# Kernel optimization log

Measured on AMD Instinct MI355X. Metric: run time of the kernel, lower is better.

## Reference

```python
import jax, jax.numpy as jnp
import numpy as np

B, S, D = 512, 81, 1024
NH, DH = 16, 64
C, H1, G, FF = 32, 256, 256, 4096


def _ln(x, g, b, eps=1e-5):
    m = x.mean(-1, keepdims=True)
    v = ((x - m) ** 2).mean(-1, keepdims=True)
    return (x - m) * jax.lax.rsqrt(v + eps) * g + b


def _mish(x):
    return x * jnp.tanh(jax.nn.softplus(x))


def setup_inputs() -> dict:
    key = jax.random.key(0)
    ks = iter(jax.random.split(key, 32))
    n = lambda shape, s=0.02: jax.random.normal(next(ks), shape, jnp.float32) * s
    return {
        "x": jax.random.normal(next(ks), (B, S, D), jnp.float32),
        "w_compress": n((D, C)), "b_compress": jnp.zeros((C,)),
        "w_d1": n((S * C, H1)), "b_d1": jnp.zeros((H1,)),
        "ln1s_g": jnp.ones((H1,)), "ln1s_b": jnp.zeros((H1,)),
        "w_d2": n((H1, NH * G)), "b_d2": jnp.zeros((NH * G,)),
        "ln2s_g": jnp.ones((NH * G,)), "ln2s_b": jnp.zeros((NH * G,)),
        "w_gg": n((G, S * S)), "b_gg": jnp.zeros((S * S,)),
        "wq": n((D, D)), "bq": jnp.zeros((D,)),
        "wk": n((D, D)), "bk": jnp.zeros((D,)),
        "wv": n((D, D)), "bv": jnp.zeros((D,)),
        "wo": n((D, D)), "bo": jnp.zeros((D,)),
        "ln1_g": jnp.ones((D,)), "ln1_b": jnp.zeros((D,)),
        "w_f1": n((D, FF)), "b_f1": jnp.zeros((FF,)),
        "w_f2": n((FF, D)), "b_f2": jnp.zeros((D,)),
        "fln_g": jnp.ones((D,)), "fln_b": jnp.zeros((D,)),
    }


def reference(x, w_compress, b_compress, w_d1, b_d1, ln1s_g, ln1s_b,
              w_d2, b_d2, ln2s_g, ln2s_b, w_gg, b_gg,
              wq, bq, wk, bk, wv, bv, wo, bo, ln1_g, ln1_b,
              w_f1, b_f1, w_f2, b_f2, fln_g, fln_b):
    b = x.shape[0]
    # --- Smolgen: per-position attention bias ---
    h = jax.nn.silu(x @ w_compress + b_compress).reshape(b, S * C)
    h = jax.nn.silu(_ln(h @ w_d1 + b_d1, ln1s_g, ln1s_b))
    h = jax.nn.silu(_ln(h @ w_d2 + b_d2, ln2s_g, ln2s_b))
    h = h.reshape(b, NH, G)
    smol_bias = (h @ w_gg + b_gg).reshape(b, NH, S, S)
    # --- Attention with additive bias ---
    q = (x @ wq + bq).reshape(b, S, NH, DH)
    k = (x @ wk + bk).reshape(b, S, NH, DH)
    v = (x @ wv + bv).reshape(b, S, NH, DH)
    scores = jnp.einsum("bqhd,bkhd->bhqk", q, k) / np.sqrt(DH) + smol_bias
    attn = jax.nn.softmax(scores, axis=-1)
    out = jnp.einsum("bhqk,bkhd->bqhd", attn, v).reshape(b, S, D)
    h = _ln(out @ wo + bo + x, ln1_g, ln1_b)
    # --- FFN ---
    f = _mish(h @ w_f1 + b_f1)
    return _ln(f @ w_f2 + b_f2 + h, fln_g, fln_b)
```

## Files before the change

kernel.cpp:

```cpp
#include <hip/hip_runtime.h>
#include <hip/hip_bf16.h>
#include <cstdint>
#include <cstdio>

using bf16 = __hip_bfloat16;
typedef __attribute__((ext_vector_type(8))) short bf16x8;
typedef __attribute__((ext_vector_type(4))) float f32x4;

__device__ __forceinline__ void gload_lds16(const void* g, void* l) {
  __builtin_amdgcn_global_load_lds((__attribute__((address_space(1))) void*)g,
                                   (__attribute__((address_space(3))) void*)l,
                                   16, 0, 0);
}

__device__ __forceinline__ float bfu2f(unsigned short u) {
  return __uint_as_float((unsigned int)u << 16);
}
__device__ __forceinline__ unsigned short f2bfu(float f) {
  bf16 b = __float2bfloat16(f);
  return *(unsigned short*)&b;
}

enum { EP_NONE = 0, EP_SILU = 1, EP_MISH = 2, EP_RES = 3, EP_RESB = 4 };

template<int EPI>
__global__ __launch_bounds__(512, 1)
void gemm256(const bf16* __restrict__ A, const bf16* __restrict__ Bt,
             int N, int Nb, int K, int gx,
             const float* __restrict__ bias,
             const float* __restrict__ residf,
             const bf16* __restrict__ residb,
             bf16* __restrict__ outb)
{
  __shared__ char lds[131072];
  const int tid  = threadIdx.x;
  const int lane = tid & 63;
  const int wid  = tid >> 6;
  const int wm = wid >> 2, wn = wid & 3;
  const int lr = lane & 15, kg = lane >> 4;

  const int nwg = gridDim.x;
  const int q8 = nwg >> 3, r8 = nwg & 7;
  const int xcd = blockIdx.x & 7, idx = blockIdx.x >> 3;
  const int wg2 = (xcd < r8 ? xcd * (q8 + 1) : r8 * (q8 + 1) + (xcd - r8) * q8) + idx;
  const int bx = wg2 % gx, by = wg2 / gx;
  const long brow = (long)bx * 256, bcol = (long)by * 256;

  const size_t rb = (size_t)K * 2;
  const int r0   = wid * 8 + (lane >> 3);
  const int coff = ((lane & 7) ^ (lane >> 3)) << 4;
  const char* aS = (const char*)A  + (size_t)(brow + r0) * rb + coff;
  const char* bS = (const char*)Bt + (size_t)(bcol + r0) * rb + coff;
  char* ldsA = lds;
  char* ldsB = lds + 65536;
  const int luni = wid * 1024;

  const int ktiles = K >> 6;

  auto stageA = [&](int t, int q) {
    gload_lds16(aS + (size_t)t * 128 + (size_t)q * 64 * rb,
                ldsA + (t & 1) * 32768 + q * 8192 + luni);
  };
  auto stageB = [&](int t, int q) {
    gload_lds16(bS + (size_t)t * 128 + (size_t)q * 64 * rb,
                ldsB + (t & 1) * 32768 + q * 8192 + luni);
  };

  f32x4 acc[8][4] = {};

  stageA(0, 0); stageA(0, 2); stageB(0, 0); stageB(0, 1);
  stageB(0, 2); stageB(0, 3); stageA(0, 1); stageA(0, 3);
  if (ktiles > 1) { stageA(1, 0); stageA(1, 2); stageB(1, 0); stageB(1, 1); }

  const int swz   = (lr & 7) << 4;
  const int kb0   = (kg << 4) ^ swz;
  const int kb1   = ((4 + kg) << 4) ^ swz;
  const int abase = (wm * 128 + lr) * 128;
  const int bbase = (wn * 64 + lr) * 128;

  for (int t = 0; t < ktiles; ++t) {
    const char* pA = ldsA + (t & 1) * 32768;
    const char* pB = ldsB + (t & 1) * 32768;
    bf16x8 af[4], b0[4], b1[4];

    if (t + 1 < ktiles) asm volatile("s_waitcnt vmcnt(4)" ::: "memory");
    else                asm volatile("s_waitcnt vmcnt(0)" ::: "memory");
    __builtin_amdgcn_s_barrier();
    __builtin_amdgcn_sched_barrier(0);
#pragma unroll
    for (int i = 0; i < 4; i++) af[i] = *(const bf16x8*)(pA + abase + i * 2048 + kb0);
#pragma unroll
    for (int j = 0; j < 4; j++) b0[j] = *(const bf16x8*)(pB + bbase + j * 2048 + kb0);
    if (t + 1 < ktiles) { stageB(t + 1, 2); stageB(t + 1, 3); }
    __builtin_amdgcn_s_barrier();
    asm volatile("s_waitcnt lgkmcnt(0)" ::: "memory");
    __builtin_amdgcn_sched_barrier(0);
    __builtin_amdgcn_s_setprio(1);
#pragma unroll
    for (int i = 0; i < 4; i++)
#pragma unroll
      for (int j = 0; j < 4; j++)
        acc[i][j] = __builtin_amdgcn_mfma_f32_16x16x32_bf16(af[i], b0[j], acc[i][j], 0, 0, 0);
    __builtin_amdgcn_s_setprio(0);
    __builtin_amdgcn_s_barrier();

#pragma unroll
    for (int i = 0; i < 4; i++) af[i] = *(const bf16x8*)(pA + abase + i * 2048 + kb1);
#pragma unroll
    for (int j = 0; j < 4; j++) b1[j] = *(const bf16x8*)(pB + bbase + j * 2048 + kb1);
    if (t + 1 < ktiles) { stageA(t + 1, 1); stageA(t + 1, 3); }
    __builtin_amdgcn_s_barrier();
    asm volatile("s_waitcnt lgkmcnt(0)" ::: "memory");
    __builtin_amdgcn_sched_barrier(0);
    __builtin_amdgcn_s_setprio(1);
#pragma unroll
    for (int i = 0; i < 4; i++)
#pragma unroll
      for (int j = 0; j < 4; j++)
        acc[i][j] = __builtin_amdgcn_mfma_f32_16x16x32_bf16(af[i], b1[j], acc[i][j], 0, 0, 0);
    __builtin_amdgcn_s_setprio(0);
    __builtin_amdgcn_s_barrier();

#pragma unroll
    for (int i = 0; i < 4; i++) af[i] = *(const bf16x8*)(pA + abase + (i + 4) * 2048 + kb0);
    if (t + 2 < ktiles) { stageA(t + 2, 0); stageA(t + 2, 2); }
    __builtin_amdgcn_s_barrier();
    asm volatile("s_waitcnt lgkmcnt(0)" ::: "memory");
    __builtin_amdgcn_sched_barrier(0);
    __builtin_amdgcn_s_setprio(1);
#pragma unroll
    for (int i = 0; i < 4; i++)
#pragma unroll
      for (int j = 0; j < 4; j++)
        acc[i + 4][j] = __builtin_amdgcn_mfma_f32_16x16x32_bf16(af[i], b0[j], acc[i + 4][j], 0, 0, 0);
    __builtin_amdgcn_s_setprio(0);
    __builtin_amdgcn_s_barrier();

#pragma unroll
    for (int i = 0; i < 4; i++) af[i] = *(const bf16x8*)(pA + abase + (i + 4) * 2048 + kb1);
    if (t + 2 < ktiles) { stageB(t + 2, 0); stageB(t + 2, 1); }
    __builtin_amdgcn_s_barrier();
    asm volatile("s_waitcnt lgkmcnt(0)" ::: "memory");
    __builtin_amdgcn_sched_barrier(0);
    __builtin_amdgcn_s_setprio(1);
#pragma unroll
    for (int i = 0; i < 4; i++)
#pragma unroll
      for (int j = 0; j < 4; j++)
        acc[i + 4][j] = __builtin_amdgcn_mfma_f32_16x16x32_bf16(af[i], b1[j], acc[i + 4][j], 0, 0, 0);
    __builtin_amdgcn_s_setprio(0);
    __builtin_amdgcn_s_barrier();
  }

  char* lC = lds;
  const int cr = kg * 4;
#pragma unroll
  for (int j = 0; j < 4; j++) {
    const int tcol = wn * 64 + j * 16 + lr;
    const long gcol = bcol + tcol;
    const float bv = (gcol < Nb) ? bias[gcol] : 0.f;
#pragma unroll
    for (int i = 0; i < 8; i++) {
#pragma unroll
      for (int r = 0; r < 4; r++) {
        const int row = wm * 128 + i * 16 + cr + r;
        float v = acc[i][j][r] + bv;
        if constexpr (EPI == EP_MISH) {
          float e = __expf(fminf(v, 20.f));
          float u = (1.f + e); u *= u;
          v = v * (u - 1.f) / (u + 1.f);
        }
        *(unsigned short*)(lC + row * 512 + ((tcol * 2) ^ ((row & 12) << 3))) = f2bfu(v);
      }
    }
  }
  __syncthreads();
  const int trow = tid >> 5;
  const int tcb  = (tid & 31) * 16;
#pragma unroll
  for (int it = 0; it < 16; ++it) {
    const int row = it * 16 + trow;
    bf16x8 vv = *(const bf16x8*)(lC + row * 512 + (tcb ^ ((row & 12) << 3)));
    const long grow = brow + row;
    bf16* dst = outb + grow * (long)N + bcol + (tcb >> 1);
    if constexpr (EPI == EP_RES) {
      const float* rs = residf + grow * (long)N + bcol + (tcb >> 1);
      float4 ra = *(const float4*)rs, rb2 = *(const float4*)(rs + 4);
      float rv[8] = {ra.x, ra.y, ra.z, ra.w, rb2.x, rb2.y, rb2.z, rb2.w};
      bf16x8 ov;
#pragma unroll
      for (int e = 0; e < 8; e++)
        ov[e] = (short)f2bfu(bfu2f((unsigned short)vv[e]) + rv[e]);
      *(bf16x8*)dst = ov;
    } else if constexpr (EPI == EP_RESB) {
      bf16x8 rb3 = *(const bf16x8*)(residb + grow * (long)N + bcol + (tcb >> 1));
      bf16x8 ov;
#pragma unroll
      for (int e = 0; e < 8; e++)
        ov[e] = (short)f2bfu(bfu2f((unsigned short)vv[e]) + bfu2f((unsigned short)rb3[e]));
      *(bf16x8*)dst = ov;
    } else {
      *(bf16x8*)dst = vv;
    }
  }
}

template<int EPI, bool OUTF>
__global__ __launch_bounds__(256)
void gemm_kernel(const bf16* __restrict__ A, const bf16* __restrict__ Bt,
                 int M, int N, int K,
                 const float* __restrict__ bias,
                 const float* __restrict__ residf,
                 const bf16* __restrict__ residb,
                 float* __restrict__ outf, bf16* __restrict__ outb)
{
  __shared__ bf16 lA[128 * 32];
  __shared__ bf16 lB[128 * 32];
  const int tid  = threadIdx.x;
  const int lane = tid & 63;
  const int wvid = tid >> 6;
  const int wr = (wvid >> 1) * 64;
  const int wc = (wvid & 1) * 64;
  const long brow = (long)blockIdx.x * 128;
  const long bcol = (long)blockIdx.y * 128;
  const int lr = lane & 15;
  const int k8 = (lane >> 4) * 8;

  const int lofs0 = wvid * 1024;
  const int lofs1 = lofs0 + 4096;
  const int o0 = lofs0 + lane * 16;
  const int o1 = o0 + 4096;
  const int r0 = o0 >> 6, c0 = o0 & 63;
  const int r1 = o1 >> 6, c1 = o1 & 63;

  f32x4 acc[4][4] = {};

  for (int k0 = 0; k0 < K; k0 += 32) {
    const long kb = (long)k0 * 2;
    gload_lds16((const char*)A  + ((brow + r0) * (long)K) * 2 + kb + c0, (char*)lA + lofs0);
    gload_lds16((const char*)A  + ((brow + r1) * (long)K) * 2 + kb + c1, (char*)lA + lofs1);
    gload_lds16((const char*)Bt + ((bcol + r0) * (long)K) * 2 + kb + c0, (char*)lB + lofs0);
    gload_lds16((const char*)Bt + ((bcol + r1) * (long)K) * 2 + kb + c1, (char*)lB + lofs1);
    __syncthreads();
    bf16x8 af[4], bf_[4];
#pragma unroll
    for (int i = 0; i < 4; i++)
      af[i] = *(const bf16x8*)&lA[(wr + i * 16 + lr) * 32 + k8];
#pragma unroll
    for (int j = 0; j < 4; j++)
      bf_[j] = *(const bf16x8*)&lB[(wc + j * 16 + lr) * 32 + k8];
#pragma unroll
    for (int i = 0; i < 4; i++)
#pragma unroll
      for (int j = 0; j < 4; j++)
        acc[i][j] = __builtin_amdgcn_mfma_f32_16x16x32_bf16(af[i], bf_[j], acc[i][j], 0, 0, 0);
    __syncthreads();
  }

  const int cr = (lane >> 4) * 4;
  const int cc = lane & 15;
#pragma unroll
  for (int j = 0; j < 4; j++) {
    const long col = bcol + wc + j * 16 + cc;
    if (col >= N) continue;
    const float bv = bias[col];
#pragma unroll
    for (int i = 0; i < 4; i++) {
#pragma unroll
      for (int r = 0; r < 4; r++) {
        const long row = brow + wr + i * 16 + cr + r;
        float v = acc[i][j][r] + bv;
        if constexpr (EPI == EP_RES)  v += residf[row * N + col];
        if constexpr (EPI == EP_RESB) v += __bfloat162float(residb[row * N + col]);
        if constexpr (EPI == EP_SILU) v = v / (1.f + __expf(-v));
        if constexpr (EPI == EP_MISH) {
          float t = __expf(fminf(v, 20.f));
          float u = (1.f + t); u *= u;
          v = v * (u - 1.f) / (u + 1.f);
        }
        if constexpr (OUTF) outf[row * N + col] = v;
        else                outb[row * N + col] = __float2bfloat16(v);
      }
    }
  }
}

__global__ __launch_bounds__(256)
void transpose_to_bf16(const float* __restrict__ W, bf16* __restrict__ Bt,
                       int K, int N, int Npad)
{
  __shared__ float tile[32][33];
  const int n0 = blockIdx.x * 32, k0 = blockIdx.y * 32;
  const int tx = threadIdx.x, ty = threadIdx.y;
  for (int r = ty; r < 32; r += 8) {
    int k = k0 + r, n = n0 + tx;
    tile[r][tx] = (k < K && n < N) ? W[(size_t)k * N + n] : 0.f;
  }
  __syncthreads();
  for (int r = ty; r < 32; r += 8) {
    int n = n0 + r, k = k0 + tx;
    if (n < Npad && k < K) Bt[(size_t)n * K + k] = __float2bfloat16(tile[tx][r]);
  }
}

__global__ __launch_bounds__(256)
void cvt_f32_bf16(const float* __restrict__ in, bf16* __restrict__ out, long n)
{
  long i = ((long)blockIdx.x * 256 + threadIdx.x) * 4;
  const long stride = (long)gridDim.x * 256 * 4;
  for (; i < n; i += stride) {
    float4 v = *(const float4*)(in + i);
    out[i]     = __float2bfloat16(v.x);
    out[i + 1] = __float2bfloat16(v.y);
    out[i + 2] = __float2bfloat16(v.z);
    out[i + 3] = __float2bfloat16(v.w);
  }
}

__global__ __launch_bounds__(256)
void pack3(const float* __restrict__ a, const float* __restrict__ b,
           const float* __restrict__ c, float* __restrict__ o, int n)
{
  int i = blockIdx.x * 256 + threadIdx.x;
  if (i < n) { o[i] = a[i]; o[n + i] = b[i]; o[2 * n + i] = c[i]; }
}

template<int ACT>
__global__ __launch_bounds__(256)
void ln_rows(const float* __restrict__ inf, const float* __restrict__ g,
             const float* __restrict__ be, bf16* __restrict__ ob, int C)
{
  const long row = blockIdx.x;
  float s = 0.f, ss = 0.f;
  for (int c = threadIdx.x; c < C; c += 256) {
    float v = inf[row * C + c];
    s += v; ss += v * v;
  }
#pragma unroll
  for (int o = 32; o; o >>= 1) { s += __shfl_xor(s, o); ss += __shfl_xor(ss, o); }
  __shared__ float p1[4], p2[4];
  const int wv = threadIdx.x >> 6;
  if ((threadIdx.x & 63) == 0) { p1[wv] = s; p2[wv] = ss; }
  __syncthreads();
  s  = p1[0] + p1[1] + p1[2] + p1[3];
  ss = p2[0] + p2[1] + p2[2] + p2[3];
  const float mean = s / C;
  const float var  = ss / C - mean * mean;
  const float rstd = rsqrtf(var + 1e-5f);
  for (int c = threadIdx.x; c < C; c += 256) {
    float v = (inf[row * C + c] - mean) * rstd * g[c] + be[c];
    if (ACT == 1) v = v / (1.f + __expf(-v));
    ob[row * C + c] = __float2bfloat16(v);
  }
}

template<bool WF, bool WB>
__global__ __launch_bounds__(256)
void ln1024(const bf16* __restrict__ inb, const float* __restrict__ g,
            const float* __restrict__ be, float* __restrict__ of,
            bf16* __restrict__ ob)
{
  const size_t row = blockIdx.x;
  const int t = threadIdx.x;
  const unsigned short* xr = (const unsigned short*)(inb + row * 1024) + t * 4;
  ushort4 raw = *(const ushort4*)xr;
  float v0 = bfu2f(raw.x), v1 = bfu2f(raw.y), v2 = bfu2f(raw.z), v3 = bfu2f(raw.w);
  float s = v0 + v1 + v2 + v3;
  float ss = v0 * v0 + v1 * v1 + v2 * v2 + v3 * v3;
#pragma unroll
  for (int o = 32; o; o >>= 1) { s += __shfl_xor(s, o); ss += __shfl_xor(ss, o); }
  __shared__ float p1[4], p2[4];
  const int wv = t >> 6;
  if ((t & 63) == 0) { p1[wv] = s; p2[wv] = ss; }
  __syncthreads();
  s  = p1[0] + p1[1] + p1[2] + p1[3];
  ss = p2[0] + p2[1] + p2[2] + p2[3];
  const float mean = s * (1.f / 1024.f);
  const float var  = ss * (1.f / 1024.f) - mean * mean;
  const float rstd = rsqrtf(var + 1e-5f);
  const int c = t * 4;
  float4 gg = *(const float4*)(g + c);
  float4 bb = *(const float4*)(be + c);
  float y0 = (v0 - mean) * rstd * gg.x + bb.x;
  float y1 = (v1 - mean) * rstd * gg.y + bb.y;
  float y2 = (v2 - mean) * rstd * gg.z + bb.z;
  float y3 = (v3 - mean) * rstd * gg.w + bb.w;
  if (WF) *(float4*)(of + row * 1024 + c) = make_float4(y0, y1, y2, y3);
  if (WB) {
    ushort4 o4 = { f2bfu(y0), f2bfu(y1), f2bfu(y2), f2bfu(y3) };
    *(ushort4*)((unsigned short*)(ob + row * 1024) + t * 4) = o4;
  }
}

__global__ __launch_bounds__(384)
void attn_mfma(const bf16* __restrict__ qkv, const bf16* __restrict__ smol,
               bf16* __restrict__ out)
{
  __shared__ char smem[37888];
  char* lqc = smem;
  char* lkc = smem + 12288;
  short* lvt = (short*)(smem + 24576);
  char* lpc = smem;

  const int b = blockIdx.x, h = blockIdx.y;
  const int tid = threadIdx.x;
  const int lane = tid & 63;
  const int w = tid >> 6;
  const int lr = lane & 15;
  const int kg = lane >> 4;

  const size_t qkv_base = (size_t)(b * 81) * 3072 + h * 64;

  for (int idx = tid; idx < 1296; idx += 384) {
    int which = idx >= 648;
    int e = which ? idx - 648 : idx;
    int s = e >> 3, c = e & 7;
    bf16x8 v = *(const bf16x8*)(qkv + qkv_base + (size_t)s * 3072 + which * 1024 + c * 8);
    char* base = which ? lkc : lqc;
    *(bf16x8*)(base + s * 128 + ((c ^ (s & 7)) << 4)) = v;
  }
  for (int idx = tid; idx < 648; idx += 384) {
    int s = idx >> 3, c = idx & 7;
    bf16x8 v = *(const bf16x8*)(qkv + qkv_base + (size_t)s * 3072 + 2048 + c * 8);
#pragma unroll
    for (int j = 0; j < 8; j++) lvt[(c * 8 + j) * 104 + s] = v[j];
  }
  {
    bf16x8 z = {};
    for (int idx = tid; idx < 240; idx += 384) {
      int which = idx >= 120;
      int e = which ? idx - 120 : idx;
      int s = 81 + (e >> 3), c = e & 7;
      char* base = which ? lkc : lqc;
      *(bf16x8*)(base + s * 128 + ((c ^ (s & 7)) << 4)) = z;
    }
    for (int idx = tid; idx < 1472; idx += 384) {
      int d = idx / 23, s = 81 + idx % 23;
      lvt[d * 104 + s] = 0;
    }
  }
  __syncthreads();

  f32x4 sacc[6] = {};
  const int m = w * 16 + lr;
#pragma unroll
  for (int ks = 0; ks < 2; ks++) {
    bf16x8 af = *(const bf16x8*)(lqc + m * 128 + ((((ks << 2) + kg) ^ (m & 7)) << 4));
#pragma unroll
    for (int j = 0; j < 6; j++) {
      int n = j * 16 + lr;
      bf16x8 bf_ = *(const bf16x8*)(lkc + n * 128 + ((((ks << 2) + kg) ^ (n & 7)) << 4));
      sacc[j] = __builtin_amdgcn_mfma_f32_16x16x32_bf16(af, bf_, sacc[j], 0, 0, 0);
    }
  }

  const bf16* smrow = smol + (size_t)(b * 16 + h) * 6656;
  float p[6][4];
#pragma unroll
  for (int j = 0; j < 6; j++) {
    int col = j * 16 + lr;
#pragma unroll
    for (int r = 0; r < 4; r++) {
      int row = w * 16 + kg * 4 + r;
      float sv = sacc[j][r] * 0.125f;
      if (col < 81) {
        if (row < 81) sv += __bfloat162float(smrow[row * 81 + col]);
      } else sv = -3.0e38f;
      p[j][r] = sv;
    }
  }
#pragma unroll
  for (int r = 0; r < 4; r++) {
    float mx = p[0][r];
#pragma unroll
    for (int j = 1; j < 6; j++) mx = fmaxf(mx, p[j][r]);
    mx = fmaxf(mx, __shfl_xor(mx, 1)); mx = fmaxf(mx, __shfl_xor(mx, 2));
    mx = fmaxf(mx, __shfl_xor(mx, 4)); mx = fmaxf(mx, __shfl_xor(mx, 8));
    float sum = 0.f;
#pragma unroll
    for (int j = 0; j < 6; j++) { float e = __expf(p[j][r] - mx); p[j][r] = e; sum += e; }
    sum += __shfl_xor(sum, 1); sum += __shfl_xor(sum, 2);
    sum += __shfl_xor(sum, 4); sum += __shfl_xor(sum, 8);
    float inv = 1.f / sum;
#pragma unroll
    for (int j = 0; j < 6; j++) p[j][r] *= inv;
  }
  __syncthreads();

#pragma unroll
  for (int j = 0; j < 6; j++) {
    int col = j * 16 + lr;
#pragma unroll
    for (int r = 0; r < 4; r++) {
      int row = w * 16 + kg * 4 + r;
      *(unsigned short*)(lpc + row * 256 + ((((col >> 3) ^ (row & 7)) << 4)) + (col & 7) * 2)
          = f2bfu(p[j][r]);
    }
  }
  __syncthreads();

  f32x4 oacc[4] = {};
#pragma unroll
  for (int ks = 0; ks < 3; ks++) {
    bf16x8 pa = *(const bf16x8*)(lpc + m * 256 + ((((ks << 2) + kg) ^ (m & 7)) << 4));
#pragma unroll
    for (int j2 = 0; j2 < 4; j2++) {
      int n = j2 * 16 + lr;
      bf16x8 vb = *(const bf16x8*)((char*)lvt + n * 208 + ((ks << 2) + kg) * 16);
      oacc[j2] = __builtin_amdgcn_mfma_f32_16x16x32_bf16(pa, vb, oacc[j2], 0, 0, 0);
    }
  }
#pragma unroll
  for (int j2 = 0; j2 < 4; j2++) {
    int d = j2 * 16 + lr;
#pragma unroll
    for (int r = 0; r < 4; r++) {
      int row = w * 16 + kg * 4 + r;
      if (row < 81)
        out[(size_t)(b * 81 + row) * 1024 + h * 64 + d] = __float2bfloat16(oacc[j2][r]);
    }
  }
}

extern "C" void kernel_launch(void* const* d_in, const int* in_sizes, int n_in,
                              void* d_out, int out_size, void* d_ws, size_t ws_size,
                              hipStream_t stream)
{
  const float* x     = (const float*)d_in[0];
  const float* w_c   = (const float*)d_in[1];
  const float* b_c   = (const float*)d_in[2];
  const float* w_d1  = (const float*)d_in[3];
  const float* b_d1  = (const float*)d_in[4];
  const float* ln1sg = (const float*)d_in[5];
  const float* ln1sb = (const float*)d_in[6];
  const float* w_d2  = (const float*)d_in[7];
  const float* b_d2  = (const float*)d_in[8];
  const float* ln2sg = (const float*)d_in[9];
  const float* ln2sb = (const float*)d_in[10];
  const float* w_gg  = (const float*)d_in[11];
  const float* b_gg  = (const float*)d_in[12];
  const float* wq    = (const float*)d_in[13];
  const float* bq    = (const float*)d_in[14];
  const float* wk    = (const float*)d_in[15];
  const float* bk    = (const float*)d_in[16];
  const float* wvp   = (const float*)d_in[17];
  const float* bv    = (const float*)d_in[18];
  const float* wo    = (const float*)d_in[19];
  const float* bo    = (const float*)d_in[20];
  const float* ln1g  = (const float*)d_in[21];
  const float* ln1b  = (const float*)d_in[22];
  const float* w_f1  = (const float*)d_in[23];
  const float* b_f1  = (const float*)d_in[24];
  const float* w_f2  = (const float*)d_in[25];
  const float* b_f2  = (const float*)d_in[26];
  const float* flng  = (const float*)d_in[27];
  const float* flnb  = (const float*)d_in[28];
  float* out = (float*)d_out;

  char* ws = (char*)d_ws;
  size_t off = 0;
  auto alloc = [&](size_t bytes) -> char* {
    char* p = ws + off; off += (bytes + 255) & ~(size_t)255; return p;
  };
  bf16*  Bt_c  = (bf16*)alloc(262144);
  bf16*  Bt_d1 = (bf16*)alloc(1327104);
  bf16*  Bt_d2 = (bf16*)alloc(2097152);
  bf16*  Bt_gg = (bf16*)alloc(3407872);
  bf16*  Bt_qkv= (bf16*)alloc(6291456);
  bf16*  Bt_wo = (bf16*)alloc(2097152);
  bf16*  Bt_f1 = (bf16*)alloc(8388608);
  bf16*  Bt_f2 = (bf16*)alloc(8388608);
  float* bqkv  = (float*)alloc(12288);
  bf16*  h0b   = (bf16*)alloc(2654208);
  float* pre_s = (float*)alloc(8388608);
  bf16*  h1b   = (bf16*)alloc(262144);
  bf16*  h2b   = (bf16*)alloc(4194304);
  char*  S1    = alloc(84934656);
  char*  S2    = alloc(339738624);
  char*  S3    = alloc(109051904);

  bf16* xb     = (bf16*)S1;
  bf16* hmidb  = (bf16*)S1;
  bf16* qkvb   = (bf16*)S2;
  bf16* aob    = (bf16*)(S2 + 254803968);
  bf16* fb     = (bf16*)S2;
  bf16* smol   = (bf16*)S3;
  bf16* preln1 = (bf16*)S3;
  bf16* preln2 = (bf16*)S3;

  if (ws_size < off) { printf("WS too small: %zu < %zu\n", ws_size, off); return; }

  const dim3 tb(32, 8);
  transpose_to_bf16<<<dim3(4, 32),   tb, 0, stream>>>(w_c,  Bt_c,  1024, 32,   128);
  transpose_to_bf16<<<dim3(8, 81),   tb, 0, stream>>>(w_d1, Bt_d1, 2592, 256,  256);
  transpose_to_bf16<<<dim3(128, 8),  tb, 0, stream>>>(w_d2, Bt_d2, 256,  4096, 4096);
  transpose_to_bf16<<<dim3(208, 8),  tb, 0, stream>>>(w_gg, Bt_gg, 256,  6561, 6656);
  transpose_to_bf16<<<dim3(32, 32),  tb, 0, stream>>>(wq,   Bt_qkv,             1024, 1024, 1024);
  transpose_to_bf16<<<dim3(32, 32),  tb, 0, stream>>>(wk,   Bt_qkv + 1024*1024, 1024, 1024, 1024);
  transpose_to_bf16<<<dim3(32, 32),  tb, 0, stream>>>(wvp,  Bt_qkv + 2048*1024, 1024, 1024, 1024);
  transpose_to_bf16<<<dim3(32, 32),  tb, 0, stream>>>(wo,   Bt_wo, 1024, 1024, 1024);
  transpose_to_bf16<<<dim3(128, 32), tb, 0, stream>>>(w_f1, Bt_f1, 1024, 4096, 4096);
  transpose_to_bf16<<<dim3(32, 128), tb, 0, stream>>>(w_f2, Bt_f2, 4096, 1024, 1024);
  pack3<<<4, 256, 0, stream>>>(bq, bk, bv, bqkv, 1024);
  cvt_f32_bf16<<<2048, 256, 0, stream>>>(x, xb, 42467328L);

  gemm_kernel<EP_SILU, false><<<dim3(324, 1), 256, 0, stream>>>(
      xb, Bt_c, 41472, 32, 1024, b_c, nullptr, nullptr, nullptr, h0b);
  gemm_kernel<EP_NONE, true><<<dim3(4, 2), 256, 0, stream>>>(
      h0b, Bt_d1, 512, 256, 2592, b_d1, nullptr, nullptr, pre_s, nullptr);
  ln_rows<1><<<512, 256, 0, stream>>>(pre_s, ln1sg, ln1sb, h1b, 256);
  gemm_kernel<EP_NONE, true><<<dim3(4, 32), 256, 0, stream>>>(
      h1b, Bt_d2, 512, 4096, 256, b_d2, nullptr, nullptr, pre_s, nullptr);
  ln_rows<1><<<512, 256, 0, stream>>>(pre_s, ln2sg, ln2sb, h2b, 4096);
  gemm256<EP_NONE><<<32 * 26, 512, 0, stream>>>(
      h2b, Bt_gg, 6656, 6561, 256, 32, b_gg, nullptr, nullptr, smol);

  gemm256<EP_NONE><<<162 * 12, 512, 0, stream>>>(
      xb, Bt_qkv, 3072, 3072, 1024, 162, bqkv, nullptr, nullptr, qkvb);
  attn_mfma<<<dim3(512, 16), 384, 0, stream>>>(qkvb, smol, aob);
  gemm256<EP_RESB><<<162 * 4, 512, 0, stream>>>(
      aob, Bt_wo, 1024, 1024, 1024, 162, bo, nullptr, xb, preln1);
  ln1024<false, true><<<41472, 256, 0, stream>>>(preln1, ln1g, ln1b, nullptr, hmidb);

  gemm256<EP_MISH><<<162 * 16, 512, 0, stream>>>(
      hmidb, Bt_f1, 4096, 4096, 1024, 162, b_f1, nullptr, nullptr, fb);
  gemm256<EP_RESB><<<162 * 4, 512, 0, stream>>>(
      fb, Bt_f2, 1024, 1024, 4096, 162, b_f2, nullptr, hmidb, preln2);
  ln1024<true, false><<<41472, 256, 0, stream>>>(preln2, flng, flnb, out, nullptr);
}
```

Before: 1.761 ms.

## Double-buffer GEMM register fragments to overlap LDS reads with MFMA

Restructures the GEMM main loop so that LDS fragment loads for the next sub-step are issued before the current MFMA block runs, using two register sets (af0/af1, b0/b1). The first fragments are prefetched before the loop, and next-tile fragments are loaded inside the final sub-step, removing one barrier per phase. This is meant to hide LDS read latency behind matrix instructions, at the cost of more VGPR pressure and a more delicate barrier/waitcnt ordering across the double-buffered LDS stages.

```diff
diff --git a/kernel.cpp b/kernel.cpp
--- a/kernel.cpp
+++ b/kernel.cpp
@@ -67,10 +67,18 @@
   };
 
   f32x4 acc[8][4] = {};
+  bf16x8 af0[4], af1[4], b0[4], b1[4];
 
   stageA(0, 0); stageA(0, 2); stageB(0, 0); stageB(0, 1);
   stageB(0, 2); stageB(0, 3); stageA(0, 1); stageA(0, 3);
-  if (ktiles > 1) { stageA(1, 0); stageA(1, 2); stageB(1, 0); stageB(1, 1); }
+  if (ktiles > 1) {
+    stageA(1, 0); stageA(1, 2); stageB(1, 0); stageB(1, 1);
+    asm volatile("s_waitcnt vmcnt(4)" ::: "memory");
+  } else {
+    asm volatile("s_waitcnt vmcnt(0)" ::: "memory");
+  }
+  __builtin_amdgcn_s_barrier();
+  __builtin_amdgcn_sched_barrier(0);
 
   const int swz   = (lr & 7) << 4;
   const int kb0   = (kg << 4) ^ swz;
@@ -78,76 +86,80 @@
   const int abase = (wm * 128 + lr) * 128;
   const int bbase = (wn * 64 + lr) * 128;
 
+#pragma unroll
+  for (int i = 0; i < 4; i++) af0[i] = *(const bf16x8*)(ldsA + abase + i * 2048 + kb0);
+#pragma unroll
+  for (int j = 0; j < 4; j++) b0[j]  = *(const bf16x8*)(ldsB + bbase + j * 2048 + kb0);
+
   for (int t = 0; t < ktiles; ++t) {
     const char* pA = ldsA + (t & 1) * 32768;
     const char* pB = ldsB + (t & 1) * 32768;
-    bf16x8 af[4], b0[4], b1[4];
-
-    if (t + 1 < ktiles) asm volatile("s_waitcnt vmcnt(4)" ::: "memory");
-    else                asm volatile("s_waitcnt vmcnt(0)" ::: "memory");
-    __builtin_amdgcn_s_barrier();
-    __builtin_amdgcn_sched_barrier(0);
-#pragma unroll
-    for (int i = 0; i < 4; i++) af[i] = *(const bf16x8*)(pA + abase + i * 2048 + kb0);
-#pragma unroll
-    for (int j = 0; j < 4; j++) b0[j] = *(const bf16x8*)(pB + bbase + j * 2048 + kb0);
-    if (t + 1 < ktiles) { stageB(t + 1, 2); stageB(t + 1, 3); }
-    __builtin_amdgcn_s_barrier();
+
     asm volatile("s_waitcnt lgkmcnt(0)" ::: "memory");
     __builtin_amdgcn_sched_barrier(0);
+#pragma unroll
+    for (int i = 0; i < 4; i++) af1[i] = *(const bf16x8*)(pA + abase + i * 2048 + kb1);
+#pragma unroll
+    for (int j = 0; j < 4; j++) b1[j]  = *(const bf16x8*)(pB + bbase + j * 2048 + kb1);
+    if (t + 1 < ktiles) { stageB(t + 1, 2); stageB(t + 1, 3); }
     __builtin_amdgcn_s_setprio(1);
 #pragma unroll
     for (int i = 0; i < 4; i++)
 #pragma unroll
       for (int j = 0; j < 4; j++)
-        acc[i][j] = __builtin_amdgcn_mfma_f32_16x16x32_bf16(af[i], b0[j], acc[i][j], 0, 0, 0);
+        acc[i][j] = __builtin_amdgcn_mfma_f32_16x16x32_bf16(af0[i], b0[j], acc[i][j], 0, 0, 0);
     __builtin_amdgcn_s_setprio(0);
     __builtin_amdgcn_s_barrier();
 
-#pragma unroll
-    for (int i = 0; i < 4; i++) af[i] = *(const bf16x8*)(pA + abase + i * 2048 + kb1);
-#pragma unroll
-    for (int j = 0; j < 4; j++) b1[j] = *(const bf16x8*)(pB + bbase + j * 2048 + kb1);
-    if (t + 1 < ktiles) { stageA(t + 1, 1); stageA(t + 1, 3); }
-    __builtin_amdgcn_s_barrier();
     asm volatile("s_waitcnt lgkmcnt(0)" ::: "memory");
     __builtin_amdgcn_sched_barrier(0);
+#pragma unroll
+    for (int i = 0; i < 4; i++) af0[i] = *(const bf16x8*)(pA + abase + (i + 4) * 2048 + kb0);
+    if (t + 1 < ktiles) { stageA(t + 1, 1); stageA(t + 1, 3); }
     __builtin_amdgcn_s_setprio(1);
 #pragma unroll
     for (int i = 0; i < 4; i++)
 #pragma unroll
       for (int j = 0; j < 4; j++)
-        acc[i][j] = __builtin_amdgcn_mfma_f32_16x16x32_bf16(af[i], b1[j], acc[i][j], 0, 0, 0);
+        acc[i][j] = __builtin_amdgcn_mfma_f32_16x16x32_bf16(af1[i], b1[j], acc[i][j], 0, 0, 0);
     __builtin_amdgcn_s_setprio(0);
     __builtin_amdgcn_s_barrier();
 
-#pragma unroll
-    for (int i = 0; i < 4; i++) af[i] = *(const bf16x8*)(pA + abase + (i + 4) * 2048 + kb0);
-    if (t + 2 < ktiles) { stageA(t + 2, 0); stageA(t + 2, 2); }
-    __builtin_amdgcn_s_barrier();
     asm volatile("s_waitcnt lgkmcnt(0)" ::: "memory");
     __builtin_amdgcn_sched_barrier(0);
+#pragma unroll
+    for (int i = 0; i < 4; i++) af1[i] = *(const bf16x8*)(pA + abase + (i + 4) * 2048 + kb1);
+    if (t + 2 < ktiles) { stageA(t + 2, 0); stageA(t + 2, 2); }
     __builtin_amdgcn_s_setprio(1);
 #pragma unroll
     for (int i = 0; i < 4; i++)
 #pragma unroll
       for (int j = 0; j < 4; j++)
-        acc[i + 4][j] = __builtin_amdgcn_mfma_f32_16x16x32_bf16(af[i], b0[j], acc[i + 4][j], 0, 0, 0);
+        acc[i + 4][j] = __builtin_amdgcn_mfma_f32_16x16x32_bf16(af0[i], b0[j], acc[i + 4][j], 0, 0, 0);
     __builtin_amdgcn_s_setprio(0);
     __builtin_amdgcn_s_barrier();
 
-#pragma unroll
-    for (int i = 0; i < 4; i++) af[i] = *(const bf16x8*)(pA + abase + (i + 4) * 2048 + kb1);
-    if (t + 2 < ktiles) { stageB(t + 2, 0); stageB(t + 2, 1); }
-    __builtin_amdgcn_s_barrier();
     asm volatile("s_waitcnt lgkmcnt(0)" ::: "memory");
     __builtin_amdgcn_sched_barrier(0);
+    if (t + 2 < ktiles) { stageB(t + 2, 0); stageB(t + 2, 1); }
+    if (t + 1 < ktiles) {
+      if (t + 2 < ktiles) asm volatile("s_waitcnt vmcnt(4)" ::: "memory");
+      else                asm volatile("s_waitcnt vmcnt(0)" ::: "memory");
+      __builtin_amdgcn_s_barrier();
+      __builtin_amdgcn_sched_barrier(0);
+      const char* qA = ldsA + ((t + 1) & 1) * 32768;
+      const char* qB = ldsB + ((t + 1) & 1) * 32768;
+#pragma unroll
+      for (int i = 0; i < 4; i++) af0[i] = *(const bf16x8*)(qA + abase + i * 2048 + kb0);
+#pragma unroll
+      for (int j = 0; j < 4; j++) b0[j]  = *(const bf16x8*)(qB + bbase + j * 2048 + kb0);
+    }
     __builtin_amdgcn_s_setprio(1);
 #pragma unroll
     for (int i = 0; i < 4; i++)
 #pragma unroll
       for (int j = 0; j < 4; j++)
-        acc[i + 4][j] = __builtin_amdgcn_mfma_f32_16x16x32_bf16(af[i], b1[j], acc[i + 4][j], 0, 0, 0);
+        acc[i + 4][j] = __builtin_amdgcn_mfma_f32_16x16x32_bf16(af1[i], b1[j], acc[i + 4][j], 0, 0, 0);
     __builtin_amdgcn_s_setprio(0);
     __builtin_amdgcn_s_barrier();
   }
```

Result: no change. 1.731 ms (-1.7%).
